# Optimization experiments

Measured on AMD Instinct MI355X. Metric: run time of the kernel, lower is better.

The kernel has to match this reference:

```python
import math
import jax, jax.numpy as jnp
import numpy as np

D_MODEL = 1024
D_FF = 4096
NUM_EXPERTS = 8
TOP_K = 2
CAP_FACTOR = 1.0
AUX_COEF = 0.01
Z_COEF = 0.0


def setup_inputs() -> dict:
    key = jax.random.key(0)
    ks = jax.random.split(key, 6)
    x = jax.random.normal(ks[0], (4, 2048, D_MODEL), dtype=jnp.float32)
    router_w = jax.random.normal(ks[1], (D_MODEL, NUM_EXPERTS), dtype=jnp.float32) / math.sqrt(D_MODEL)
    router_b = jnp.zeros((NUM_EXPERTS,), dtype=jnp.float32)
    w1 = jax.random.normal(ks[2], (NUM_EXPERTS, D_MODEL, D_FF), dtype=jnp.float32) / math.sqrt(D_MODEL)
    w3 = jax.random.normal(ks[3], (NUM_EXPERTS, D_MODEL, D_FF), dtype=jnp.float32) / math.sqrt(D_MODEL)
    w2 = jax.random.normal(ks[4], (NUM_EXPERTS, D_FF, D_MODEL), dtype=jnp.float32) / math.sqrt(D_FF)
    return {"x": x, "router_w": router_w, "router_b": router_b, "w1": w1, "w3": w3, "w2": w2}


def reference(x, router_w, router_b, w1, w3, w2):
    b, s, d = x.shape
    E, k = NUM_EXPERTS, TOP_K
    T = b * s
    x_flat = x.reshape(T, d)

    # ---- router ----
    logits = x_flat @ router_w + router_b                      # [T, E]
    logits_f32 = logits.astype(jnp.float32)
    probs = jax.nn.softmax(logits_f32, axis=-1)                # [T, E]
    topk_p, topk_i = jax.lax.top_k(probs, k)                   # [T, k]
    topk_p = topk_p / jnp.clip(topk_p.sum(-1, keepdims=True), 1e-9)  # normalize_gates
    gate = topk_p.reshape(-1)                                  # [T*k]
    expert_idx = topk_i.reshape(-1)                            # [T*k]

    # ---- aux loss (load balance + z-loss) ----
    importance = probs.mean(axis=0)                            # [E]
    load = jnp.bincount(topk_i[:, 0], length=E).astype(jnp.float32) / T
    lb_loss = (importance * load).sum() * float(E)
    z_loss = jnp.mean(jnp.square(jax.nn.logsumexp(logits_f32, axis=-1)))
    aux_loss = (AUX_COEF * lb_loss + Z_COEF * z_loss).astype(x.dtype)

    # ---- capacity-based dispatch ----
    N = T * k
    cap = max(1, int(math.ceil(CAP_FACTOR * N / E)))
    x_rep = jnp.repeat(x_flat, k, axis=0)                      # [N, d]
    order = jnp.argsort(expert_idx)                            # stable sort by expert
    e_sorted = expert_idx[order]
    x_sorted = x_rep[order]
    g_sorted = gate[order].astype(x.dtype)
    counts = jnp.bincount(e_sorted, length=E)
    starts = jnp.concatenate([jnp.zeros((1,), counts.dtype), jnp.cumsum(counts)[:-1]])
    pos = jnp.arange(N, dtype=counts.dtype) - starts[e_sorted]   # rank within expert group
    keep = pos < cap
    slot = jnp.where(keep, e_sorted * cap + pos, E * cap)      # dropped tokens -> dump row

    buf = jnp.zeros((E * cap + 1, d), dtype=x.dtype).at[slot].set(x_sorted)
    buf = buf[: E * cap].reshape(E, cap, d)                    # [E, C, d]

    # ---- grouped SwiGLU experts ----
    h = jax.nn.silu(jnp.einsum('ecd,edf->ecf', buf, w1)) * jnp.einsum('ecd,edf->ecf', buf, w3)
    y = jnp.einsum('ecf,efd->ecd', h, w2).reshape(E * cap, d)

    # ---- combine ----
    gathered = y[jnp.minimum(slot, E * cap - 1)]
    out_sorted = jnp.where(keep[:, None], gathered, 0.0) * g_sorted[:, None]
    inv = jnp.argsort(order)
    out = out_sorted[inv].reshape(T, k, d).sum(axis=1)
    return out.reshape(b, s, d), aux_loss
```

## Files before the change

### kernel.cpp

```cpp
#include <hip/hip_runtime.h>
#include <hip/hip_bf16.h>
#include <math.h>

constexpr int kT    = 8192;
constexpr int kD    = 1024;
constexpr int kF    = 4096;
constexpr int kE    = 8;
constexpr int kN    = kT * 2;
constexpr int kCap  = 2048;
constexpr int kECap = kE * kCap;

typedef __attribute__((ext_vector_type(8))) short bf16x8;
typedef __attribute__((ext_vector_type(4))) float f32x4;

__device__ __forceinline__ void gload16(const __hip_bfloat16* g, __hip_bfloat16* l) {
  auto gp = (const __attribute__((address_space(1))) __hip_bfloat16*)g;
  auto lp = (__attribute__((address_space(3))) __hip_bfloat16*)l;
  __builtin_amdgcn_global_load_lds((const __attribute__((address_space(1))) void*)gp,
                                   (__attribute__((address_space(3))) void*)lp,
                                   16, 0, 0);
}

#define SYNC_VM(N) do { __builtin_amdgcn_sched_barrier(0); \
  asm volatile("s_waitcnt vmcnt(" #N ")" ::: "memory"); \
  __builtin_amdgcn_s_barrier(); \
  asm volatile("" ::: "memory"); } while (0)

__global__ void init_kernel(int* token_of) {
  int i = blockIdx.x * 256 + threadIdx.x;
  if (i < kECap) token_of[i] = -1;
}

__global__ __launch_bounds__(256)
void transpose64_kernel(const float* __restrict__ srcA, const float* __restrict__ srcB,
                        __hip_bfloat16* __restrict__ dstA, __hip_bfloat16* __restrict__ dstB,
                        int R, int C) {
  __shared__ float tile[64][65];
  const int zz = blockIdx.z;
  const int e = zz & 7;
  const float* src = (zz < 8) ? srcA : srcB;
  __hip_bfloat16* dst = (zz < 8) ? dstA : dstB;
  const size_t mat = (size_t)R * C;
  const float* s = src + (size_t)e * mat;
  __hip_bfloat16* d = dst + (size_t)e * mat;
  const int c0 = blockIdx.x * 64, r0 = blockIdx.y * 64;
  const int tid = threadIdx.x;

  const int lr = tid >> 4, lc4 = (tid & 15) * 4;
#pragma unroll
  for (int p = 0; p < 4; ++p) {
    int r = p * 16 + lr;
    float4 v = *(const float4*)(s + (size_t)(r0 + r) * C + c0 + lc4);
    tile[r][lc4] = v.x; tile[r][lc4 + 1] = v.y; tile[r][lc4 + 2] = v.z; tile[r][lc4 + 3] = v.w;
  }
  __syncthreads();

  const int c = tid >> 2, rc = (tid & 3) * 16;
  union { __hip_bfloat16 h[16]; bf16x8 v[2]; } o;
#pragma unroll
  for (int i = 0; i < 16; ++i) o.h[i] = __float2bfloat16(tile[rc + i][c]);
  __hip_bfloat16* drow = d + (size_t)(c0 + c) * R + r0 + rc;
  *(bf16x8*)drow = o.v[0];
  *(bf16x8*)(drow + 8) = o.v[1];
}

__global__ __launch_bounds__(256)
void router_kernel(const float* __restrict__ x, const float* __restrict__ rw,
                   const float* __restrict__ rb, int* __restrict__ e_idx,
                   float* __restrict__ gates, float* __restrict__ probs_out) {
  int t = blockIdx.x * 4 + (threadIdx.x >> 6);
  int lane = threadIdx.x & 63;
  const float* xr = x + (size_t)t * kD;
  float acc[8];
#pragma unroll
  for (int e = 0; e < 8; ++e) acc[e] = 0.f;
  for (int i = 0; i < kD / 256; ++i) {
    int d = i * 256 + lane * 4;
    float4 xv = *(const float4*)(xr + d);
#pragma unroll
    for (int j = 0; j < 4; ++j) {
      float xs = (j == 0) ? xv.x : (j == 1) ? xv.y : (j == 2) ? xv.z : xv.w;
      const float4* w4 = (const float4*)(rw + (size_t)(d + j) * 8);
      float4 wa = w4[0], wb = w4[1];
      acc[0] += xs * wa.x; acc[1] += xs * wa.y; acc[2] += xs * wa.z; acc[3] += xs * wa.w;
      acc[4] += xs * wb.x; acc[5] += xs * wb.y; acc[6] += xs * wb.z; acc[7] += xs * wb.w;
    }
  }
#pragma unroll
  for (int off = 32; off >= 1; off >>= 1) {
#pragma unroll
    for (int e = 0; e < 8; ++e) acc[e] += __shfl_xor(acc[e], off);
  }
  if (lane == 0) {
    float l[8], m = -1e30f;
#pragma unroll
    for (int e = 0; e < 8; ++e) { l[e] = acc[e] + rb[e]; m = fmaxf(m, l[e]); }
    float p[8], s = 0.f;
#pragma unroll
    for (int e = 0; e < 8; ++e) { p[e] = __expf(l[e] - m); s += p[e]; }
    float inv = 1.f / s;
#pragma unroll
    for (int e = 0; e < 8; ++e) p[e] *= inv;
    int i1 = 0;
#pragma unroll
    for (int e = 1; e < 8; ++e) if (p[e] > p[i1]) i1 = e;
    int i2 = (i1 == 0) ? 1 : 0;
#pragma unroll
    for (int e = 0; e < 8; ++e) if (e != i1 && e != i2 && p[e] > p[i2]) i2 = e;
    float den = fmaxf(p[i1] + p[i2], 1e-9f);
    e_idx[2 * t] = i1; e_idx[2 * t + 1] = i2;
    gates[2 * t] = p[i1] / den; gates[2 * t + 1] = p[i2] / den;
    float4* po = (float4*)(probs_out + (size_t)t * 8);
    po[0] = make_float4(p[0], p[1], p[2], p[3]);
    po[1] = make_float4(p[4], p[5], p[6], p[7]);
  }
}

__global__ __launch_bounds__(1024)
void aux_kernel(const float* __restrict__ probs, const int* __restrict__ e_idx,
                float* __restrict__ aux_out) {
  int tid = threadIdx.x, lane = tid & 63, wave = tid >> 6;
  float imp[8];
  int cnt[8];
#pragma unroll
  for (int e = 0; e < 8; ++e) { imp[e] = 0.f; cnt[e] = 0; }
  for (int t = tid; t < kT; t += 1024) {
    const float4* p4 = (const float4*)(probs + (size_t)t * 8);
    float4 a = p4[0], b = p4[1];
    imp[0] += a.x; imp[1] += a.y; imp[2] += a.z; imp[3] += a.w;
    imp[4] += b.x; imp[5] += b.y; imp[6] += b.z; imp[7] += b.w;
    ++cnt[e_idx[2 * t] & 7];
  }
#pragma unroll
  for (int off = 32; off >= 1; off >>= 1) {
#pragma unroll
    for (int e = 0; e < 8; ++e) {
      imp[e] += __shfl_xor(imp[e], off);
      cnt[e] += __shfl_xor(cnt[e], off);
    }
  }
  __shared__ float simp[16][8];
  __shared__ int scnt[16][8];
  if (lane == 0) {
#pragma unroll
    for (int e = 0; e < 8; ++e) { simp[wave][e] = imp[e]; scnt[wave][e] = cnt[e]; }
  }
  __syncthreads();
  if (tid == 0) {
    float lb = 0.f;
    for (int e = 0; e < 8; ++e) {
      float I = 0.f; int C = 0;
      for (int w = 0; w < 16; ++w) { I += simp[w][e]; C += scnt[w][e]; }
      lb += (I / (float)kT) * ((float)C / (float)kT);
    }
    aux_out[0] = 0.01f * lb * (float)kE;
  }
}

__global__ __launch_bounds__(256)
void rank_kernel(const int* __restrict__ e_idx, int* __restrict__ pos) {
  int e = blockIdx.x;
  __shared__ int wave_sum[4];
  __shared__ int running;
  int tid = threadIdx.x, lane = tid & 63, wave = tid >> 6;
  if (tid == 0) running = 0;
  __syncthreads();
  for (int base = 0; base < kN; base += 256) {
    int i = base + tid;
    bool f = (e_idx[i] == e);
    unsigned long long m = __ballot(f);
    int wpre = __popcll(m & ((1ull << lane) - 1ull));
    if (lane == 0) wave_sum[wave] = __popcll(m);
    __syncthreads();
    int woff = 0;
    for (int w = 0; w < wave; ++w) woff += wave_sum[w];
    int r = running;
    if (f) pos[i] = r + woff + wpre;
    __syncthreads();
    if (tid == 0) running = r + wave_sum[0] + wave_sum[1] + wave_sum[2] + wave_sum[3];
    __syncthreads();
  }
}

__global__ __launch_bounds__(256)
void scatter_kernel(const int* __restrict__ e_idx, const int* __restrict__ pos,
                    int* __restrict__ slot_of, int* __restrict__ token_of) {
  int i = blockIdx.x * 256 + threadIdx.x;
  if (i >= kN) return;
  int p = pos[i];
  if (p < kCap) {
    int slot = e_idx[i] * kCap + p;
    slot_of[i] = slot;
    token_of[slot] = i >> 1;
  } else {
    slot_of[i] = -1;
  }
}

struct __attribute__((aligned(8))) bf16x4s { __hip_bfloat16 v[4]; };

__global__ __launch_bounds__(64)
void gather_kernel(const float* __restrict__ x, const int* __restrict__ token_of,
                   __hip_bfloat16* __restrict__ buf) {
  int slot = blockIdx.x, lane = threadIdx.x;
  int t = token_of[slot];
  __hip_bfloat16* br = buf + (size_t)slot * kD;
  if (t >= 0) {
    const float* xr = x + (size_t)t * kD;
#pragma unroll
    for (int j = 0; j < 4; ++j) {
      int dd = (j * 64 + lane) * 4;
      float4 v = *(const float4*)(xr + dd);
      bf16x4s o;
      o.v[0] = __float2bfloat16(v.x); o.v[1] = __float2bfloat16(v.y);
      o.v[2] = __float2bfloat16(v.z); o.v[3] = __float2bfloat16(v.w);
      *(bf16x4s*)(br + dd) = o;
    }
  } else {
    bf16x4s z;
    z.v[0] = z.v[1] = z.v[2] = z.v[3] = __float2bfloat16(0.f);
#pragma unroll
    for (int j = 0; j < 4; ++j) *(bf16x4s*)(br + (j * 64 + lane) * 4) = z;
  }
}

__global__ __launch_bounds__(512, 2)
void gemm1_kernel(const __hip_bfloat16* __restrict__ Abase,
                  const __hip_bfloat16* __restrict__ W1t,
                  const __hip_bfloat16* __restrict__ W3t,
                  __hip_bfloat16* __restrict__ H) {
  constexpr int K = kD;
  constexpr int NT = K / 64;
  const int e = blockIdx.z, mt = blockIdx.y, ft = blockIdx.x;
  const int tid = threadIdx.x, lane = tid & 63, wave = tid >> 6;
  const int wr = wave >> 1, wc = wave & 1;
  const int frow = lane & 15, fk = lane >> 4;

  const __hip_bfloat16* A  = Abase + (size_t)(e * kCap + mt * 256) * K;
  const __hip_bfloat16* B1 = W1t + ((size_t)e * kF + ft * 128) * K;
  const __hip_bfloat16* B3 = W3t + ((size_t)e * kF + ft * 128) * K;

  extern __shared__ __hip_bfloat16 lds[];

  f32x4 accU[4][4], accV[4][4];
#pragma unroll
  for (int m = 0; m < 4; ++m)
#pragma unroll
    for (int n = 0; n < 4; ++n) {
      accU[m][n] = (f32x4){0.f, 0.f, 0.f, 0.f};
      accV[m][n] = (f32x4){0.f, 0.f, 0.f, 0.f};
    }

  auto stageA = [&](int t, int b) {
#pragma unroll
    for (int j = 0; j < 4; ++j) {
      int c = j * 128 + wc * 64 + lane;
      int rl = c >> 3, s = c & 7;
      const __hip_bfloat16* g = A + (size_t)(wr * 64 + rl) * K + t * 64 + (s ^ (rl & 7)) * 8;
      gload16(g, &lds[b * 32768 + wr * 4096 + (j * 128 + wc * 64) * 8]);
    }
  };
  auto stageB1 = [&](int t, int b) {
#pragma unroll
    for (int j = 0; j < 2; ++j) {
      int c = j * 256 + wr * 64 + lane;
      int rl = c >> 3, s = c & 7;
      const __hip_bfloat16* g = B1 + (size_t)(wc * 64 + rl) * K + t * 64 + (s ^ (rl & 7)) * 8;
      gload16(g, &lds[b * 32768 + 16384 + wc * 4096 + (j * 256 + wr * 64) * 8]);
    }
  };
  auto stageB3 = [&](int t, int b) {
#pragma unroll
    for (int j = 0; j < 2; ++j) {
      int c = j * 256 + wr * 64 + lane;
      int rl = c >> 3, s = c & 7;
      const __hip_bfloat16* g = B3 + (size_t)(wc * 64 + rl) * K + t * 64 + (s ^ (rl & 7)) * 8;
      gload16(g, &lds[b * 32768 + 16384 + 8192 + wc * 4096 + (j * 256 + wr * 64) * 8]);
    }
  };
  auto phase = [&](int b, f32x4 (&ac)[4][4], bf16x8 (&af)[4][2], int broff, bool loadA) {
    if (loadA) {
#pragma unroll
      for (int m = 0; m < 4; ++m)
#pragma unroll
        for (int h = 0; h < 2; ++h) {
          int row = wr * 64 + m * 16 + frow;
          af[m][h] = *(const bf16x8*)&lds[b * 32768 + row * 64 + ((h * 4 + fk) ^ (row & 7)) * 8];
        }
    }
    bf16x8 bf[4][2];
#pragma unroll
    for (int n = 0; n < 4; ++n)
#pragma unroll
      for (int h = 0; h < 2; ++h) {
        int row = broff + wc * 64 + n * 16 + frow;
        bf[n][h] = *(const bf16x8*)&lds[b * 32768 + 16384 + row * 64 + ((h * 4 + fk) ^ (row & 7)) * 8];
      }
    __builtin_amdgcn_s_setprio(1);
#pragma unroll
    for (int m = 0; m < 4; ++m)
#pragma unroll
      for (int n = 0; n < 4; ++n)
#pragma unroll
        for (int h = 0; h < 2; ++h)
          ac[m][n] = __builtin_amdgcn_mfma_f32_16x16x32_bf16(af[m][h], bf[n][h], ac[m][n], 0, 0, 0);
    __builtin_amdgcn_s_setprio(0);
    __builtin_amdgcn_sched_barrier(0);
  };

  stageA(0, 0); stageB1(0, 0); stageB3(0, 0);

  for (int t = 0; t < NT; ++t) {
    const int b = t & 1, nb = b ^ 1;
    const bool nx = (t + 1 < NT);
    SYNC_VM(2);
    if (nx) stageA(t + 1, nb);
    bf16x8 af[4][2];
    phase(b, accU, af, 0, true);
    if (nx) { SYNC_VM(4); } else { SYNC_VM(0); }
    if (nx) stageB1(t + 1, nb);
    phase(b, accV, af, 128, false);
    if (nx) stageB3(t + 1, nb);
  }

  __hip_bfloat16* Ht = H + (size_t)(e * kCap + mt * 256) * kF + ft * 128;
#pragma unroll
  for (int m = 0; m < 4; ++m)
#pragma unroll
    for (int n = 0; n < 4; ++n)
#pragma unroll
      for (int r = 0; r < 4; ++r) {
        int row = wr * 64 + m * 16 + fk * 4 + r;
        int col = wc * 64 + n * 16 + frow;
        float u = accU[m][n][r], v = accV[m][n][r];
        float hval = (u / (1.f + __expf(-u))) * v;
        Ht[(size_t)row * kF + col] = __float2bfloat16(hval);
      }
}

__global__ __launch_bounds__(512, 2)
void gemm2_kernel(const __hip_bfloat16* __restrict__ Hbase,
                  const __hip_bfloat16* __restrict__ W2t,
                  float* __restrict__ Y) {
  constexpr int K = kF;
  constexpr int NT = K / 64;
  const int e = blockIdx.z, mt = blockIdx.y, nt = blockIdx.x;
  const int tid = threadIdx.x, lane = tid & 63, wave = tid >> 6;
  const int wr = wave >> 2, wc = wave & 3;
  const int frow = lane & 15, fk = lane >> 4;

  const __hip_bfloat16* A = Hbase + (size_t)(e * kCap + mt * 256) * K;
  const __hip_bfloat16* B = W2t + ((size_t)e * kD + nt * 256) * K;

  extern __shared__ __hip_bfloat16 lds[];

  f32x4 acc[2][4][4];
#pragma unroll
  for (int p = 0; p < 2; ++p)
#pragma unroll
    for (int m = 0; m < 4; ++m)
#pragma unroll
      for (int n = 0; n < 4; ++n) acc[p][m][n] = (f32x4){0.f, 0.f, 0.f, 0.f};

  auto stageB = [&](int t, int b) {
#pragma unroll
    for (int j = 0; j < 4; ++j) {
      int c = j * 128 + wr * 64 + lane;
      int rl = c >> 3, s = c & 7;
      const __hip_bfloat16* g = B + (size_t)(wc * 64 + rl) * K + t * 64 + (s ^ (rl & 7)) * 8;
      gload16(g, &lds[b * 32768 + 16384 + wc * 4096 + (j * 128 + wr * 64) * 8]);
    }
  };
  auto stageA = [&](int t, int p, int b) {
    int q = 2 * wr + p;
#pragma unroll
    for (int j = 0; j < 2; ++j) {
      int c = j * 256 + wc * 64 + lane;
      int rl = c >> 3, s = c & 7;
      const __hip_bfloat16* g = A + (size_t)(q * 64 + rl) * K + t * 64 + (s ^ (rl & 7)) * 8;
      gload16(g, &lds[b * 32768 + q * 4096 + (j * 256 + wc * 64) * 8]);
    }
  };
  auto phase = [&](int b, int p, f32x4 (&ac)[4][4], bf16x8 (&bf)[4][2], bool loadB) {
    bf16x8 a[4][2];
#pragma unroll
    for (int m = 0; m < 4; ++m)
#pragma unroll
      for (int h = 0; h < 2; ++h) {
        int row = wr * 128 + p * 64 + m * 16 + frow;
        a[m][h] = *(const bf16x8*)&lds[b * 32768 + row * 64 + ((h * 4 + fk) ^ (row & 7)) * 8];
      }
    if (loadB) {
#pragma unroll
      for (int n = 0; n < 4; ++n)
#pragma unroll
        for (int h = 0; h < 2; ++h) {
          int row = wc * 64 + n * 16 + frow;
          bf[n][h] = *(const bf16x8*)&lds[b * 32768 + 16384 + row * 64 + ((h * 4 + fk) ^ (row & 7)) * 8];
        }
    }
    __builtin_amdgcn_s_setprio(1);
#pragma unroll
    for (int m = 0; m < 4; ++m)
#pragma unroll
      for (int n = 0; n < 4; ++n)
#pragma unroll
        for (int h = 0; h < 2; ++h)
          ac[m][n] = __builtin_amdgcn_mfma_f32_16x16x32_bf16(a[m][h], bf[n][h], ac[m][n], 0, 0, 0);
    __builtin_amdgcn_s_setprio(0);
    __builtin_amdgcn_sched_barrier(0);
  };

  stageB(0, 0); stageA(0, 0, 0); stageA(0, 1, 0);

  for (int t = 0; t < NT; ++t) {
    const int b = t & 1, nb = b ^ 1;
    const bool nx = (t + 1 < NT);
    SYNC_VM(2);
    if (nx) stageB(t + 1, nb);
    bf16x8 bf[4][2];
    phase(b, 0, acc[0], bf, true);
    if (nx) { SYNC_VM(4); } else { SYNC_VM(0); }
    if (nx) stageA(t + 1, 0, nb);
    phase(b, 1, acc[1], bf, false);
    if (nx) stageA(t + 1, 1, nb);
  }

  float* Yt = Y + (size_t)(e * kCap + mt * 256) * kD + nt * 256;
#pragma unroll
  for (int p = 0; p < 2; ++p)
#pragma unroll
    for (int m = 0; m < 4; ++m)
#pragma unroll
      for (int n = 0; n < 4; ++n)
#pragma unroll
        for (int r = 0; r < 4; ++r) {
          int row = wr * 128 + p * 64 + m * 16 + fk * 4 + r;
          int col = wc * 64 + n * 16 + frow;
          Yt[(size_t)row * kD + col] = acc[p][m][n][r];
        }
}

__global__ __launch_bounds__(256)
void combine_kernel(const float* __restrict__ Y, const int* __restrict__ slot_of,
                    const float* __restrict__ gates, float* __restrict__ out) {
  int t = blockIdx.x;
  int dd = threadIdx.x * 4;
  int s0 = slot_of[2 * t], s1 = slot_of[2 * t + 1];
  float g0 = gates[2 * t], g1 = gates[2 * t + 1];
  float4 r = {0.f, 0.f, 0.f, 0.f};
  if (s0 >= 0) {
    float4 v = *(const float4*)(Y + (size_t)s0 * kD + dd);
    r.x += g0 * v.x; r.y += g0 * v.y; r.z += g0 * v.z; r.w += g0 * v.w;
  }
  if (s1 >= 0) {
    float4 v = *(const float4*)(Y + (size_t)s1 * kD + dd);
    r.x += g1 * v.x; r.y += g1 * v.y; r.z += g1 * v.z; r.w += g1 * v.w;
  }
  *(float4*)(out + (size_t)t * kD + dd) = r;
}

extern "C" void kernel_launch(void* const* d_in, const int* in_sizes, int n_in,
                              void* d_out, int out_size, void* d_ws, size_t ws_size,
                              hipStream_t stream) {
  (void)in_sizes; (void)n_in; (void)out_size; (void)ws_size;
  const float* x  = (const float*)d_in[0];
  const float* rw = (const float*)d_in[1];
  const float* rb = (const float*)d_in[2];
  const float* w1 = (const float*)d_in[3];
  const float* w3 = (const float*)d_in[4];
  const float* w2 = (const float*)d_in[5];
  float* out = (float*)d_out;

  char* base = (char*)d_ws;
  size_t off = 0;
  auto alloc = [&](size_t bytes) -> char* {
    char* r = base + off;
    off += (bytes + 255) & ~(size_t)255;
    return r;
  };
  __hip_bfloat16* w1t = (__hip_bfloat16*)alloc((size_t)kE * kF * kD * 2);
  __hip_bfloat16* w3t = (__hip_bfloat16*)alloc((size_t)kE * kF * kD * 2);
  __hip_bfloat16* w2t = (__hip_bfloat16*)alloc((size_t)kE * kD * kF * 2);
  __hip_bfloat16* buf = (__hip_bfloat16*)alloc((size_t)kECap * kD * 2);
  __hip_bfloat16* h   = (__hip_bfloat16*)alloc((size_t)kECap * kF * 2);
  float*          y   = (float*)alloc((size_t)kECap * kD * 4);
  int*   e_idx    = (int*)alloc((size_t)kN * 4);
  float* gates    = (float*)alloc((size_t)kN * 4);
  int*   pos      = (int*)alloc((size_t)kN * 4);
  int*   slot_of  = (int*)alloc((size_t)kN * 4);
  int*   token_of = (int*)alloc((size_t)kECap * 4);
  float* probs    = (float*)alloc((size_t)kT * 8 * 4);

  init_kernel<<<kECap / 256, 256, 0, stream>>>(token_of);
  transpose64_kernel<<<dim3(kF / 64, kD / 64, 16), 256, 0, stream>>>(w1, w3, w1t, w3t, kD, kF);
  transpose64_kernel<<<dim3(kD / 64, kF / 64, 8), 256, 0, stream>>>(w2, w2, w2t, w2t, kF, kD);
  router_kernel<<<kT / 4, 256, 0, stream>>>(x, rw, rb, e_idx, gates, probs);
  aux_kernel<<<1, 1024, 0, stream>>>(probs, e_idx, out + (size_t)kT * kD);
  rank_kernel<<<kE, 256, 0, stream>>>(e_idx, pos);
  scatter_kernel<<<kN / 256, 256, 0, stream>>>(e_idx, pos, slot_of, token_of);
  gather_kernel<<<kECap, 64, 0, stream>>>(x, token_of, buf);
  gemm1_kernel<<<dim3(kF / 128, kCap / 256, kE), 512, 131072, stream>>>(buf, w1t, w3t, h);
  gemm2_kernel<<<dim3(kD / 256, kCap / 256, kE), 512, 131072, stream>>>(h, w2t, y);
  combine_kernel<<<kT, 256, 0, stream>>>(y, slot_of, gates, out);
}
```

Before: 617.5 us.

## Use one barrier per K-tile and prefetch the whole next tile early in expert GEMMs

Restructures the main loops of both expert GEMM kernels (the gate/up SwiGLU GEMM and the down-projection GEMM). Each K-tile now has a single wait-for-all-loads plus barrier instead of two partial-vmcnt barriers. All async global-to-LDS loads for the next tile are issued right after the first fragment reads from the current buffer. The aim is to cut barrier stalls and give the prefetch the full compute time of a tile to land. The cost is waiting on vmcnt(0) at each tile boundary and keeping more fragment registers live at once.

```diff
diff --git a/kernel.cpp b/kernel.cpp
--- a/kernel.cpp
+++ b/kernel.cpp
@@ -21,10 +21,10 @@
                                    16, 0, 0);
 }
 
-#define SYNC_VM(N) do { __builtin_amdgcn_sched_barrier(0); \
-  asm volatile("s_waitcnt vmcnt(" #N ")" ::: "memory"); \
+#define SYNC_TILE() do { __builtin_amdgcn_sched_barrier(0); \
+  asm volatile("s_waitcnt vmcnt(0)" ::: "memory"); \
   __builtin_amdgcn_s_barrier(); \
-  asm volatile("" ::: "memory"); } while (0)
+  __builtin_amdgcn_sched_barrier(0); } while (0)
 
 __global__ void init_kernel(int* token_of) {
   int i = blockIdx.x * 256 + threadIdx.x;
@@ -278,49 +278,57 @@
       gload16(g, &lds[b * 32768 + 16384 + 8192 + wc * 4096 + (j * 256 + wr * 64) * 8]);
     }
   };
-  auto phase = [&](int b, f32x4 (&ac)[4][4], bf16x8 (&af)[4][2], int broff, bool loadA) {
-    if (loadA) {
-#pragma unroll
-      for (int m = 0; m < 4; ++m)
-#pragma unroll
-        for (int h = 0; h < 2; ++h) {
-          int row = wr * 64 + m * 16 + frow;
-          af[m][h] = *(const bf16x8*)&lds[b * 32768 + row * 64 + ((h * 4 + fk) ^ (row & 7)) * 8];
-        }
-    }
-    bf16x8 bf[4][2];
-#pragma unroll
-    for (int n = 0; n < 4; ++n)
-#pragma unroll
-      for (int h = 0; h < 2; ++h) {
-        int row = broff + wc * 64 + n * 16 + frow;
-        bf[n][h] = *(const bf16x8*)&lds[b * 32768 + 16384 + row * 64 + ((h * 4 + fk) ^ (row & 7)) * 8];
-      }
-    __builtin_amdgcn_s_setprio(1);
-#pragma unroll
-    for (int m = 0; m < 4; ++m)
-#pragma unroll
-      for (int n = 0; n < 4; ++n)
-#pragma unroll
-        for (int h = 0; h < 2; ++h)
-          ac[m][n] = __builtin_amdgcn_mfma_f32_16x16x32_bf16(af[m][h], bf[n][h], ac[m][n], 0, 0, 0);
-    __builtin_amdgcn_s_setprio(0);
-    __builtin_amdgcn_sched_barrier(0);
-  };
 
   stageA(0, 0); stageB1(0, 0); stageB3(0, 0);
 
   for (int t = 0; t < NT; ++t) {
     const int b = t & 1, nb = b ^ 1;
     const bool nx = (t + 1 < NT);
-    SYNC_VM(2);
-    if (nx) stageA(t + 1, nb);
-    bf16x8 af[4][2];
-    phase(b, accU, af, 0, true);
-    if (nx) { SYNC_VM(4); } else { SYNC_VM(0); }
-    if (nx) stageB1(t + 1, nb);
-    phase(b, accV, af, 128, false);
-    if (nx) stageB3(t + 1, nb);
+    SYNC_TILE();
+
+    bf16x8 af[4][2], bu[4][2], bv[4][2];
+#pragma unroll
+    for (int m = 0; m < 4; ++m)
+#pragma unroll
+      for (int h = 0; h < 2; ++h) {
+        int row = wr * 64 + m * 16 + frow;
+        af[m][h] = *(const bf16x8*)&lds[b * 32768 + row * 64 + ((h * 4 + fk) ^ (row & 7)) * 8];
+      }
+#pragma unroll
+    for (int n = 0; n < 4; ++n)
+#pragma unroll
+      for (int h = 0; h < 2; ++h) {
+        int row = wc * 64 + n * 16 + frow;
+        bu[n][h] = *(const bf16x8*)&lds[b * 32768 + 16384 + row * 64 + ((h * 4 + fk) ^ (row & 7)) * 8];
+      }
+    if (nx) { stageA(t + 1, nb); stageB1(t + 1, nb); stageB3(t + 1, nb); }
+
+    __builtin_amdgcn_s_setprio(1);
+#pragma unroll
+    for (int m = 0; m < 4; ++m)
+#pragma unroll
+      for (int n = 0; n < 4; ++n)
+#pragma unroll
+        for (int h = 0; h < 2; ++h)
+          accU[m][n] = __builtin_amdgcn_mfma_f32_16x16x32_bf16(af[m][h], bu[n][h], accU[m][n], 0, 0, 0);
+    __builtin_amdgcn_s_setprio(0);
+
+#pragma unroll
+    for (int n = 0; n < 4; ++n)
+#pragma unroll
+      for (int h = 0; h < 2; ++h) {
+        int row = 128 + wc * 64 + n * 16 + frow;
+        bv[n][h] = *(const bf16x8*)&lds[b * 32768 + 16384 + row * 64 + ((h * 4 + fk) ^ (row & 7)) * 8];
+      }
+    __builtin_amdgcn_s_setprio(1);
+#pragma unroll
+    for (int m = 0; m < 4; ++m)
+#pragma unroll
+      for (int n = 0; n < 4; ++n)
+#pragma unroll
+        for (int h = 0; h < 2; ++h)
+          accV[m][n] = __builtin_amdgcn_mfma_f32_16x16x32_bf16(af[m][h], bv[n][h], accV[m][n], 0, 0, 0);
+    __builtin_amdgcn_s_setprio(0);
   }
 
   __hip_bfloat16* Ht = H + (size_t)(e * kCap + mt * 256) * kF + ft * 128;
@@ -381,49 +389,57 @@
       gload16(g, &lds[b * 32768 + q * 4096 + (j * 256 + wc * 64) * 8]);
     }
   };
-  auto phase = [&](int b, int p, f32x4 (&ac)[4][4], bf16x8 (&bf)[4][2], bool loadB) {
-    bf16x8 a[4][2];
-#pragma unroll
-    for (int m = 0; m < 4; ++m)
-#pragma unroll
-      for (int h = 0; h < 2; ++h) {
-        int row = wr * 128 + p * 64 + m * 16 + frow;
-        a[m][h] = *(const bf16x8*)&lds[b * 32768 + row * 64 + ((h * 4 + fk) ^ (row & 7)) * 8];
-      }
-    if (loadB) {
-#pragma unroll
-      for (int n = 0; n < 4; ++n)
-#pragma unroll
-        for (int h = 0; h < 2; ++h) {
-          int row = wc * 64 + n * 16 + frow;
-          bf[n][h] = *(const bf16x8*)&lds[b * 32768 + 16384 + row * 64 + ((h * 4 + fk) ^ (row & 7)) * 8];
-        }
-    }
-    __builtin_amdgcn_s_setprio(1);
-#pragma unroll
-    for (int m = 0; m < 4; ++m)
-#pragma unroll
-      for (int n = 0; n < 4; ++n)
-#pragma unroll
-        for (int h = 0; h < 2; ++h)
-          ac[m][n] = __builtin_amdgcn_mfma_f32_16x16x32_bf16(a[m][h], bf[n][h], ac[m][n], 0, 0, 0);
-    __builtin_amdgcn_s_setprio(0);
-    __builtin_amdgcn_sched_barrier(0);
-  };
 
   stageB(0, 0); stageA(0, 0, 0); stageA(0, 1, 0);
 
   for (int t = 0; t < NT; ++t) {
     const int b = t & 1, nb = b ^ 1;
     const bool nx = (t + 1 < NT);
-    SYNC_VM(2);
-    if (nx) stageB(t + 1, nb);
-    bf16x8 bf[4][2];
-    phase(b, 0, acc[0], bf, true);
-    if (nx) { SYNC_VM(4); } else { SYNC_VM(0); }
-    if (nx) stageA(t + 1, 0, nb);
-    phase(b, 1, acc[1], bf, false);
-    if (nx) stageA(t + 1, 1, nb);
+    SYNC_TILE();
+
+    bf16x8 bf[4][2], a0[4][2], a1[4][2];
+#pragma unroll
+    for (int n = 0; n < 4; ++n)
+#pragma unroll
+      for (int h = 0; h < 2; ++h) {
+        int row = wc * 64 + n * 16 + frow;
+        bf[n][h] = *(const bf16x8*)&lds[b * 32768 + 16384 + row * 64 + ((h * 4 + fk) ^ (row & 7)) * 8];
+      }
+#pragma unroll
+    for (int m = 0; m < 4; ++m)
+#pragma unroll
+      for (int h = 0; h < 2; ++h) {
+        int row = wr * 128 + m * 16 + frow;
+        a0[m][h] = *(const bf16x8*)&lds[b * 32768 + row * 64 + ((h * 4 + fk) ^ (row & 7)) * 8];
+      }
+    if (nx) { stageB(t + 1, nb); stageA(t + 1, 0, nb); stageA(t + 1, 1, nb); }
+
+    __builtin_amdgcn_s_setprio(1);
+#pragma unroll
+    for (int m = 0; m < 4; ++m)
+#pragma unroll
+      for (int n = 0; n < 4; ++n)
+#pragma unroll
+        for (int h = 0; h < 2; ++h)
+          acc[0][m][n] = __builtin_amdgcn_mfma_f32_16x16x32_bf16(a0[m][h], bf[n][h], acc[0][m][n], 0, 0, 0);
+    __builtin_amdgcn_s_setprio(0);
+
+#pragma unroll
+    for (int m = 0; m < 4; ++m)
+#pragma unroll
+      for (int h = 0; h < 2; ++h) {
+        int row = wr * 128 + 64 + m * 16 + frow;
+        a1[m][h] = *(const bf16x8*)&lds[b * 32768 + row * 64 + ((h * 4 + fk) ^ (row & 7)) * 8];
+      }
+    __builtin_amdgcn_s_setprio(1);
+#pragma unroll
+    for (int m = 0; m < 4; ++m)
+#pragma unroll
+      for (int n = 0; n < 4; ++n)
+#pragma unroll
+        for (int h = 0; h < 2; ++h)
+          acc[1][m][n] = __builtin_amdgcn_mfma_f32_16x16x32_bf16(a1[m][h], bf[n][h], acc[1][m][n], 0, 0, 0);
+    __builtin_amdgcn_s_setprio(0);
   }
 
   float* Yt = Y + (size_t)(e * kCap + mt * 256) * kD + nt * 256;
```

New measurement: 624.6 us. Within noise of the previous version (+1.2%).

## Fuse combine into gemm2 epilogue via gated atomic adds and fold scatter into rank

Applied to the files above, without the earlier changes.

The gemm2 epilogue now scales each output row by its gate and atomically adds it into the final output at the token's row. This removes the fp32 Y intermediate and the separate combine kernel. The scatter kernel is merged into rank_kernel, which writes token_of and a per-slot gate directly. init_kernel now also zeroes the output buffer. Both GEMM main loops also get an unroll-2 pragma. The cost is contention from float atomics and nondeterministic summation order across the two experts.

```diff
diff --git a/kernel.cpp b/kernel.cpp
--- a/kernel.cpp
+++ b/kernel.cpp
@@ -26,8 +26,9 @@
   __builtin_amdgcn_s_barrier(); \
   asm volatile("" ::: "memory"); } while (0)
 
-__global__ void init_kernel(int* token_of) {
+__global__ void init_kernel(int* token_of, float4* outz) {
   int i = blockIdx.x * 256 + threadIdx.x;
+  outz[i] = make_float4(0.f, 0.f, 0.f, 0.f);
   if (i < kECap) token_of[i] = -1;
 }
 
@@ -158,7 +159,8 @@
 }
 
 __global__ __launch_bounds__(256)
-void rank_kernel(const int* __restrict__ e_idx, int* __restrict__ pos) {
+void rank_kernel(const int* __restrict__ e_idx, const float* __restrict__ gates,
+                 int* __restrict__ token_of, float* __restrict__ gate_slot) {
   int e = blockIdx.x;
   __shared__ int wave_sum[4];
   __shared__ int running;
@@ -175,25 +177,16 @@
     int woff = 0;
     for (int w = 0; w < wave; ++w) woff += wave_sum[w];
     int r = running;
-    if (f) pos[i] = r + woff + wpre;
+    if (f) {
+      int p = r + woff + wpre;
+      if (p < kCap) {
+        token_of[e * kCap + p] = i >> 1;
+        gate_slot[e * kCap + p] = gates[i];
+      }
+    }
     __syncthreads();
     if (tid == 0) running = r + wave_sum[0] + wave_sum[1] + wave_sum[2] + wave_sum[3];
     __syncthreads();
-  }
-}
-
-__global__ __launch_bounds__(256)
-void scatter_kernel(const int* __restrict__ e_idx, const int* __restrict__ pos,
-                    int* __restrict__ slot_of, int* __restrict__ token_of) {
-  int i = blockIdx.x * 256 + threadIdx.x;
-  if (i >= kN) return;
-  int p = pos[i];
-  if (p < kCap) {
-    int slot = e_idx[i] * kCap + p;
-    slot_of[i] = slot;
-    token_of[slot] = i >> 1;
-  } else {
-    slot_of[i] = -1;
   }
 }
 
@@ -310,6 +303,7 @@
 
   stageA(0, 0); stageB1(0, 0); stageB3(0, 0);
 
+#pragma unroll 2
   for (int t = 0; t < NT; ++t) {
     const int b = t & 1, nb = b ^ 1;
     const bool nx = (t + 1 < NT);
@@ -341,7 +335,8 @@
 __global__ __launch_bounds__(512, 2)
 void gemm2_kernel(const __hip_bfloat16* __restrict__ Hbase,
                   const __hip_bfloat16* __restrict__ W2t,
-                  float* __restrict__ Y) {
+                  const int* __restrict__ token_of, const float* __restrict__ gate_slot,
+                  float* __restrict__ out) {
   constexpr int K = kF;
   constexpr int NT = K / 64;
   const int e = blockIdx.z, mt = blockIdx.y, nt = blockIdx.x;
@@ -413,6 +408,7 @@
 
   stageB(0, 0); stageA(0, 0, 0); stageA(0, 1, 0);
 
+#pragma unroll 2
   for (int t = 0; t < NT; ++t) {
     const int b = t & 1, nb = b ^ 1;
     const bool nx = (t + 1 < NT);
@@ -426,38 +422,33 @@
     if (nx) stageA(t + 1, 1, nb);
   }
 
-  float* Yt = Y + (size_t)(e * kCap + mt * 256) * kD + nt * 256;
+  __syncthreads();
+  int* s_tok = (int*)lds;
+  float* s_gate = (float*)((char*)lds + 1024);
+  if (tid < 256) {
+    int slot = e * kCap + mt * 256 + tid;
+    s_tok[tid] = token_of[slot];
+    s_gate[tid] = gate_slot[slot];
+  }
+  __syncthreads();
+
+  const int colbase = nt * 256 + wc * 64;
 #pragma unroll
   for (int p = 0; p < 2; ++p)
 #pragma unroll
     for (int m = 0; m < 4; ++m)
 #pragma unroll
-      for (int n = 0; n < 4; ++n)
-#pragma unroll
-        for (int r = 0; r < 4; ++r) {
-          int row = wr * 128 + p * 64 + m * 16 + fk * 4 + r;
-          int col = wc * 64 + n * 16 + frow;
-          Yt[(size_t)row * kD + col] = acc[p][m][n][r];
+      for (int r = 0; r < 4; ++r) {
+        int lrow = wr * 128 + p * 64 + m * 16 + fk * 4 + r;
+        int tkn = s_tok[lrow];
+        if (tkn >= 0) {
+          float g = s_gate[lrow];
+          float* orow = out + (size_t)tkn * kD + colbase;
+#pragma unroll
+          for (int n = 0; n < 4; ++n)
+            atomicAdd(orow + n * 16 + frow, g * acc[p][m][n][r]);
         }
-}
-
-__global__ __launch_bounds__(256)
-void combine_kernel(const float* __restrict__ Y, const int* __restrict__ slot_of,
-                    const float* __restrict__ gates, float* __restrict__ out) {
-  int t = blockIdx.x;
-  int dd = threadIdx.x * 4;
-  int s0 = slot_of[2 * t], s1 = slot_of[2 * t + 1];
-  float g0 = gates[2 * t], g1 = gates[2 * t + 1];
-  float4 r = {0.f, 0.f, 0.f, 0.f};
-  if (s0 >= 0) {
-    float4 v = *(const float4*)(Y + (size_t)s0 * kD + dd);
-    r.x += g0 * v.x; r.y += g0 * v.y; r.z += g0 * v.z; r.w += g0 * v.w;
-  }
-  if (s1 >= 0) {
-    float4 v = *(const float4*)(Y + (size_t)s1 * kD + dd);
-    r.x += g1 * v.x; r.y += g1 * v.y; r.z += g1 * v.z; r.w += g1 * v.w;
-  }
-  *(float4*)(out + (size_t)t * kD + dd) = r;
+      }
 }
 
 extern "C" void kernel_launch(void* const* d_in, const int* in_sizes, int n_in,
@@ -484,23 +475,19 @@
   __hip_bfloat16* w2t = (__hip_bfloat16*)alloc((size_t)kE * kD * kF * 2);
   __hip_bfloat16* buf = (__hip_bfloat16*)alloc((size_t)kECap * kD * 2);
   __hip_bfloat16* h   = (__hip_bfloat16*)alloc((size_t)kECap * kF * 2);
-  float*          y   = (float*)alloc((size_t)kECap * kD * 4);
   int*   e_idx    = (int*)alloc((size_t)kN * 4);
   float* gates    = (float*)alloc((size_t)kN * 4);
-  int*   pos      = (int*)alloc((size_t)kN * 4);
-  int*   slot_of  = (int*)alloc((size_t)kN * 4);
   int*   token_of = (int*)alloc((size_t)kECap * 4);
+  float* gate_slot= (float*)alloc((size_t)kECap * 4);
   float* probs    = (float*)alloc((size_t)kT * 8 * 4);
 
-  init_kernel<<<kECap / 256, 256, 0, stream>>>(token_of);
+  init_kernel<<<8192, 256, 0, stream>>>(token_of, (float4*)out);
   transpose64_kernel<<<dim3(kF / 64, kD / 64, 16), 256, 0, stream>>>(w1, w3, w1t, w3t, kD, kF);
   transpose64_kernel<<<dim3(kD / 64, kF / 64, 8), 256, 0, stream>>>(w2, w2, w2t, w2t, kF, kD);
   router_kernel<<<kT / 4, 256, 0, stream>>>(x, rw, rb, e_idx, gates, probs);
   aux_kernel<<<1, 1024, 0, stream>>>(probs, e_idx, out + (size_t)kT * kD);
-  rank_kernel<<<kE, 256, 0, stream>>>(e_idx, pos);
-  scatter_kernel<<<kN / 256, 256, 0, stream>>>(e_idx, pos, slot_of, token_of);
+  rank_kernel<<<kE, 256, 0, stream>>>(e_idx, gates, token_of, gate_slot);
   gather_kernel<<<kECap, 64, 0, stream>>>(x, token_of, buf);
   gemm1_kernel<<<dim3(kF / 128, kCap / 256, kE), 512, 131072, stream>>>(buf, w1t, w3t, h);
-  gemm2_kernel<<<dim3(kD / 256, kCap / 256, kE), 512, 131072, stream>>>(h, w2t, y);
-  combine_kernel<<<kT, 256, 0, stream>>>(y, slot_of, gates, out);
-}
+  gemm2_kernel<<<dim3(kD / 256, kCap / 256, kE), 512, 131072, stream>>>(h, w2t, token_of, gate_slot, out);
+}
```

After: 679.2 us. +10.0%, slower.
